# Kernel tuning notes

Measured on AMD Instinct MI355X. Metric: run time of the kernel, lower is better.

The kernel has to match this reference:

```python
import jax, jax.numpy as jnp
import numpy as np

N = 50000   # nodes
E = 300000  # directed edges
IN = 512
H = 256
OUT = 256
K = 4096    # K_target; since K < N, pooled node count Kc == K statically


def setup_inputs() -> dict:
    key = jax.random.key(0)
    ks = jax.random.split(key, 8)
    x = jax.random.normal(ks[0], (N, IN), jnp.float32)
    edge_index = jax.random.randint(ks[1], (2, E), 0, N)
    W1 = jax.random.normal(ks[2], (IN, H), jnp.float32) / np.float32(np.sqrt(IN))
    b1 = jnp.zeros((H,), jnp.float32)
    W2 = jax.random.normal(ks[3], (H, OUT), jnp.float32) / np.float32(np.sqrt(H))
    b2 = jnp.zeros((OUT,), jnp.float32)
    w_score = jax.random.normal(ks[4], (H,), jnp.float32) / np.float32(np.sqrt(H))
    W_skip = jax.random.normal(ks[5], (H, OUT), jnp.float32) / np.float32(np.sqrt(H))
    b_skip = jnp.zeros((OUT,), jnp.float32)
    return dict(x=x, edge_index=edge_index, W1=W1, b1=b1, W2=W2, b2=b2,
                w_score=w_score, W_skip=W_skip, b_skip=b_skip)


def _gcn_sparse(x, src, dst, W, b, n):
    # PyG GCNConv(add_self_loops=True, normalize=True): out = D^{-1/2}(A+I)D^{-1/2} x W + b,
    # degrees computed on dst after adding self loops.
    h = x @ W
    loop = jnp.arange(n)
    s = jnp.concatenate([src, loop])
    d = jnp.concatenate([dst, loop])
    deg = jax.ops.segment_sum(jnp.ones_like(d, h.dtype), d, num_segments=n)
    dinv = jnp.where(deg > 0, jax.lax.rsqrt(deg), 0.0)
    coef = (dinv[s] * dinv[d])[:, None]
    return jax.ops.segment_sum(h[s] * coef, d, num_segments=n) + b


def _forward(x, edge_index, W1, b1, W2, b2, w_score, W_skip, b_skip):
    n = x.shape[0]
    src, dst = edge_index[0], edge_index[1]

    # conv1 + relu (dropout is identity in eval mode)
    x1 = jax.nn.relu(_gcn_sparse(x, src, dst, W1, b1, n))
    raw = x1 @ w_score                       # [N] score (Linear, no bias)
    x1g = x1 * jnp.tanh(raw)[:, None]        # gated features

    # top-K node selection
    _, kept = jax.lax.top_k(raw, K)          # sorted descending, like torch.topk
    keep_mask = jnp.zeros((n,), bool).at[kept].set(True)
    deg = jax.ops.segment_sum(jnp.ones((src.shape[0],), jnp.int32), src, num_segments=n)

    # cluster ids: kept nodes get 0..K-1 in topk order
    cid = jnp.full((n,), -1, jnp.int32).at[kept].set(jnp.arange(K, dtype=jnp.int32))

    # non-kept nodes join the kept (undirected) neighbor with max degree;
    # encode (degree, -node_id) so segment_max picks max degree, tie-break smallest id
    s_all = jnp.concatenate([src, dst])
    t_all = jnp.concatenate([dst, src])
    cand = jnp.where(keep_mask[t_all], deg[t_all] * n + (n - 1 - t_all), -1)
    best = jax.ops.segment_max(cand, s_all, num_segments=n)  # empty segs -> int min
    has = best >= 0
    best_t = (n - 1) - jnp.where(has, best % n, 0)
    # global fallback: kept node with max degree (tie-break: earliest in topk order)
    enc_k = deg[kept] * K + (K - 1 - jnp.arange(K))
    bg = kept[jnp.argmax(enc_k)]
    cid = jnp.where(keep_mask, cid, jnp.where(has, cid[best_t], cid[bg]))

    # mean pooling per cluster (pool_by_partition)
    sums = jax.ops.segment_sum(x1g, cid, num_segments=K)
    cnt = jnp.maximum(jax.ops.segment_sum(jnp.ones((n,), x.dtype), cid, num_segments=K), 1.0)
    xp = sums / cnt[:, None]

    # pooled edges with dedup + self-pair removal, as dense KxK adjacency (rows = dst)
    cu, cv = cid[src], cid[dst]
    A = jnp.zeros((K, K), x.dtype).at[cv, cu].max((cu != cv).astype(x.dtype))
    Ahat = A + jnp.eye(K, dtype=x.dtype)
    di = jax.lax.rsqrt(Ahat.sum(axis=1))     # deg >= 1 from self loops
    An = di[:, None] * Ahat * di[None, :]

    # conv2 on pooled graph, broadcast back, skip connection
    xp2 = An @ (xp @ W2) + b2
    return xp2[cid] + x1 @ W_skip + b_skip


def reference(x, edge_index, W1, b1, W2, b2, w_score, W_skip, b_skip):
    return _forward(x, edge_index, W1, b1, W2, b2, w_score, W_skip, b_skip)
```

## Files before the change

### kernel.cpp

```cpp
#include <hip/hip_runtime.h>
#include <hip/hip_bf16.h>

#define N_NODES 50000
#define E_EDGES 300000
#define IN_F 512
#define H_F 256
#define OUT_F 256
#define K_CL 4096
#define KW (K_CL / 32)
#define PCH 128
#define THRESH 192
#define MAXH 1024
#define NSPL 32
#define NB2 ((N_NODES + 255) / 256)

typedef short bh8 __attribute__((ext_vector_type(8)));
typedef float f4 __attribute__((ext_vector_type(4)));
typedef unsigned short u16;

__device__ __forceinline__ unsigned fkey(float f) {
    unsigned u = __float_as_uint(f);
    return (u & 0x80000000u) ? ~u : (u | 0x80000000u);
}

__device__ __forceinline__ u16 f2bf(float f) {
    __hip_bfloat16 b = __float2bfloat16(f);
    return *reinterpret_cast<u16*>(&b);
}

__global__ __launch_bounds__(256) void init_nodes(int* cntD, int* degS,
                                                  unsigned long long* best_enc,
                                                  int* bgnode, int* heavycnt,
                                                  unsigned long long* bestpack) {
    int i = blockIdx.x * blockDim.x + threadIdx.x;
    if (i < N_NODES) { cntD[i] = 0; degS[i] = 0; best_enc[i] = 0ULL; }
    if (i == 0) { *heavycnt = 0; *bgnode = 0x7FFFFFFF; *bestpack = 0ULL; }
}

__global__ __launch_bounds__(256) void deg_edges(const int* __restrict__ src,
                                                 const int* __restrict__ dst,
                                                 int* cntD, int* degS) {
    int e = blockIdx.x * blockDim.x + threadIdx.x;
    if (e >= E_EDGES) return;
    atomicAdd(&cntD[dst[e]], 1);
    atomicAdd(&degS[src[e]], 1);
}

#define SBM 64
#define SBN 128
#define SBK 16
#define SAPAD 4
__global__ __launch_bounds__(256) void gemm_f32s(const float* __restrict__ A,
                                                 const float* __restrict__ B,
                                                 float* __restrict__ C,
                                                 int M, int Nc, int Kd) {
    __shared__ float As[2][SBK][SBM + SAPAD];
    __shared__ float Bs[2][SBK][SBN];
    int tid = threadIdx.x;
    int tx = tid & 15;
    int ty = tid >> 4;
    int lane = tid & 63;
    int wave = tid >> 6;
    int row0 = blockIdx.y * SBM, col0 = blockIdx.x * SBN;
    float acc[4][8] = {};

    int ar = tid >> 2;
    int akq = tid & 3;

    auto stage_B = [&](int k0, int bb) {
        #pragma unroll
        for (int u = 0; u < 2; ++u) {
            int chunk = wave * 2 + u;
            int krow = chunk * 2 + (lane >> 5);
            const float* gsrc = &B[(long)(k0 + krow) * Nc + col0 + (lane & 31) * 4];
            __builtin_amdgcn_global_load_lds(
                (const __attribute__((address_space(1))) void*)gsrc,
                (__attribute__((address_space(3))) void*)&Bs[bb][chunk * 2][0],
                16, 0, 0);
        }
    };
    auto stage_A = [&](int k0, int bb) {
        int gr = row0 + ar;
        float4 v = {0.f, 0.f, 0.f, 0.f};
        if (gr < M) v = *(const float4*)&A[(long)gr * Kd + k0 + akq * 4];
        As[bb][akq * 4 + 0][ar] = v.x;
        As[bb][akq * 4 + 1][ar] = v.y;
        As[bb][akq * 4 + 2][ar] = v.z;
        As[bb][akq * 4 + 3][ar] = v.w;
    };
    auto compute = [&](int bb) {
        #pragma unroll
        for (int k = 0; k < SBK; ++k) {
            float4 a0 = *(const float4*)&As[bb][k][ty * 4];
            float4 b0 = *(const float4*)&Bs[bb][k][tx * 4];
            float4 b1 = *(const float4*)&Bs[bb][k][tx * 4 + 64];
            float av[4] = {a0.x, a0.y, a0.z, a0.w};
            float bv[8] = {b0.x, b0.y, b0.z, b0.w, b1.x, b1.y, b1.z, b1.w};
            #pragma unroll
            for (int i = 0; i < 4; ++i)
                #pragma unroll
                for (int j = 0; j < 8; ++j)
                    acc[i][j] += av[i] * bv[j];
        }
    };

    stage_B(0, 0);
    stage_A(0, 0);
    __syncthreads();
    int nt = Kd / SBK;
    for (int t = 0; t < nt; ++t) {
        int cb = t & 1;
        if (t + 1 < nt) {
            stage_B(SBK * (t + 1), cb ^ 1);
            stage_A(SBK * (t + 1), cb ^ 1);
        }
        compute(cb);
        __syncthreads();
    }

    #pragma unroll
    for (int i = 0; i < 4; ++i) {
        int gr = row0 + ty * 4 + i;
        if (gr >= M) continue;
        float4 o0 = {acc[i][0], acc[i][1], acc[i][2], acc[i][3]};
        float4 o1 = {acc[i][4], acc[i][5], acc[i][6], acc[i][7]};
        *(float4*)&C[(long)gr * Nc + col0 + tx * 4] = o0;
        *(float4*)&C[(long)gr * Nc + col0 + 64 + tx * 4] = o1;
    }
}

__global__ __launch_bounds__(256) void pack_W2(const float* __restrict__ Wa, u16* Bpa,
                                               const float* __restrict__ Wb, u16* Bpb) {
    int k = blockIdx.x & 255;
    const float* W = (blockIdx.x < 256) ? Wa : Wb;
    u16* Bp = (blockIdx.x < 256) ? Bpa : Bpb;
    int col = threadIdx.x;
    int kb = k >> 5, g = (k >> 3) & 3, j = k & 7;
    Bp[(((long)(kb * 4 + g) * 256) + col) * 8 + j] = f2bf(W[(long)k * 256 + col]);
}

__global__ __launch_bounds__(256) void gemm_mfma(const u16* __restrict__ Ab,
                                                 const float* __restrict__ Af32,
                                                 const int* __restrict__ cnt,
                                                 const u16* __restrict__ Bp,
                                                 float* __restrict__ C,
                                                 int M,
                                                 const int* __restrict__ cid,
                                                 const float* __restrict__ xp2,
                                                 const float* __restrict__ bskip) {
    int tid = threadIdx.x;
    int w = tid >> 6, l = tid & 63;
    int lo16 = l & 15, hi4 = l >> 4;
    int arow = blockIdx.x * 64 + w * 16 + lo16;
    f4 acc[16];
    #pragma unroll
    for (int n = 0; n < 16; ++n) acc[n] = (f4){0.f, 0.f, 0.f, 0.f};

    float s = 1.f;
    if (Af32 && arow < M) s = 1.f / fmaxf((float)cnt[arow], 1.f);

    #pragma unroll
    for (int kb = 0; kb < 8; ++kb) {
        bh8 a = {0, 0, 0, 0, 0, 0, 0, 0};
        if (arow < M) {
            if (Af32) {
                float4 v0 = *(const float4*)&Af32[(long)arow * 256 + kb * 32 + hi4 * 8];
                float4 v1 = *(const float4*)&Af32[(long)arow * 256 + kb * 32 + hi4 * 8 + 4];
                u16 tmp[8] = {f2bf(v0.x * s), f2bf(v0.y * s), f2bf(v0.z * s), f2bf(v0.w * s),
                              f2bf(v1.x * s), f2bf(v1.y * s), f2bf(v1.z * s), f2bf(v1.w * s)};
                a = *(const bh8*)tmp;
            } else {
                a = *(const bh8*)&Ab[(long)arow * 256 + kb * 32 + hi4 * 8];
            }
        }
        const u16* bbase = &Bp[(((long)(kb * 4 + hi4)) * 256 + lo16) * 8];
        #pragma unroll
        for (int n = 0; n < 16; ++n) {
            bh8 b = *(const bh8*)&bbase[(long)n * 128];
            acc[n] = __builtin_amdgcn_mfma_f32_16x16x32_bf16(a, b, acc[n], 0, 0, 0);
        }
    }

    int orow0 = blockIdx.x * 64 + w * 16 + hi4 * 4;
    #pragma unroll
    for (int r = 0; r < 4; ++r) {
        int gr = orow0 + r;
        if (gr >= M) continue;
        long rb = (long)gr * 256;
        const float* xrow = cid ? (xp2 + (long)cid[gr] * 256) : nullptr;
        #pragma unroll
        for (int n = 0; n < 16; ++n) {
            int gc = n * 16 + lo16;
            float v = acc[n][r];
            if (cid) v += xrow[gc] + bskip[gc];
            C[rb + gc] = v;
        }
    }
}

__global__ __launch_bounds__(256) void scan_l1(const int* __restrict__ cnt,
                                               int* bsum, int n, float* dinv) {
    __shared__ int s[256];
    int t = threadIdx.x;
    int i = blockIdx.x * 256 + t;
    int v = (i < n) ? cnt[i] : 0;
    if (dinv && i < n) dinv[i] = rsqrtf((float)v + 1.0f);
    s[t] = v;
    __syncthreads();
    for (int off = 128; off > 0; off >>= 1) {
        if (t < off) s[t] += s[t + off];
        __syncthreads();
    }
    if (t == 0) bsum[blockIdx.x] = s[0];
}

__global__ __launch_bounds__(256) void scan_l2(const int* __restrict__ bsum,
                                               int* bstart, int nb) {
    __shared__ int s[256];
    int t = threadIdx.x;
    int v = (t < nb) ? bsum[t] : 0;
    s[t] = v;
    __syncthreads();
    for (int off = 1; off < 256; off <<= 1) {
        int a = (t >= off) ? s[t - off] : 0;
        __syncthreads();
        s[t] += a;
        __syncthreads();
    }
    if (t < nb) bstart[t] = s[t] - v;
}

__global__ __launch_bounds__(256) void scan_l3(const int* __restrict__ cnt,
                                               const int* __restrict__ bstart,
                                               int* start, int* cur, int n) {
    __shared__ int s[256];
    int t = threadIdx.x;
    int i = blockIdx.x * 256 + t;
    int v = (i < n) ? cnt[i] : 0;
    s[t] = v;
    __syncthreads();
    for (int off = 1; off < 256; off <<= 1) {
        int a = (t >= off) ? s[t - off] : 0;
        __syncthreads();
        s[t] += a;
        __syncthreads();
    }
    int st = bstart[blockIdx.x] + s[t] - v;
    if (i < n) { start[i] = st; cur[i] = st; }
    if (i == n - 1) start[n] = st + v;
}

__global__ __launch_bounds__(256) void csr_scatter(const int* __restrict__ src,
                                                   const int* __restrict__ dst,
                                                   int* cur, int* csr) {
    int e = blockIdx.x * blockDim.x + threadIdx.x;
    if (e >= E_EDGES) return;
    int d = dst[e];
    int p = atomicAdd(&cur[d], 1);
    csr[p] = src[e];
}

__global__ __launch_bounds__(256) void agg_fused(const float* __restrict__ h,
                                                 const float* __restrict__ dinv,
                                                 const int* __restrict__ rowptr,
                                                 const int* __restrict__ csr,
                                                 const float* __restrict__ b1,
                                                 const float* __restrict__ w_score,
                                                 float* x1, u16* x1b, float* raw) {
    __shared__ int s_src[128];
    __shared__ float s_cf[128];
    __shared__ float red[256];
    int i = blockIdx.x, j = threadIdx.x;
    float di_ = dinv[i];
    float acc = di_ * di_ * h[(long)i * H_F + j];
    int p0 = rowptr[i], p1 = rowptr[i + 1];
    for (int base = p0; base < p1; base += 128) {
        int m = p1 - base; if (m > 128) m = 128;
        if (j < m) { int s = csr[base + j]; s_src[j] = s; s_cf[j] = dinv[s]; }
        __syncthreads();
        #pragma unroll 4
        for (int t = 0; t < m; ++t)
            acc += (s_cf[t] * di_) * h[(long)s_src[t] * H_F + j];
        __syncthreads();
    }
    float v = fmaxf(acc + b1[j], 0.f);
    x1[(long)i * H_F + j] = v;
    x1b[(long)i * H_F + j] = f2bf(v);
    red[j] = v * w_score[j];
    __syncthreads();
    for (int off = 128; off > 0; off >>= 1) {
        if (j < off) red[j] += red[j + off];
        __syncthreads();
    }
    if (j == 0) raw[i] = red[0];
}

__global__ __launch_bounds__(1024) void topk_select(const float* __restrict__ raw,
                                                    unsigned* outT, int* outNeedEq) {
    __shared__ unsigned hist[256];
    __shared__ unsigned sh_prefix;
    __shared__ int sh_k;
    int tid = threadIdx.x;
    if (tid == 0) { sh_prefix = 0; sh_k = K_CL; }
    __syncthreads();
    for (int byte = 3; byte >= 0; --byte) {
        if (tid < 256) hist[tid] = 0;
        __syncthreads();
        unsigned prefix = sh_prefix;
        unsigned known_mask = (byte == 3) ? 0u : (0xFFFFFFFFu << ((byte + 1) * 8));
        for (int i = tid; i < N_NODES; i += 1024) {
            unsigned key = fkey(raw[i]);
            if ((key & known_mask) == prefix)
                atomicAdd(&hist[(key >> (byte * 8)) & 255], 1u);
        }
        __syncthreads();
        if (tid == 0) {
            int kk = sh_k;
            int cum = 0;
            int v = 255;
            for (; v > 0; --v) {
                int c = (int)hist[v];
                if (cum + c >= kk) break;
                cum += c;
            }
            sh_prefix = prefix | ((unsigned)v << (byte * 8));
            sh_k = kk - cum;
        }
        __syncthreads();
    }
    if (tid == 0) { *outT = sh_prefix; *outNeedEq = sh_k; }
}

__global__ __launch_bounds__(256) void topk_count(const float* __restrict__ raw,
                                                  const unsigned* pT,
                                                  int* bGt, int* bEq) {
    __shared__ int sg[256], se[256];
    unsigned T = *pT;
    int t = threadIdx.x;
    int i = blockIdx.x * 256 + t;
    int gt = 0, eq = 0;
    if (i < N_NODES) {
        unsigned k = fkey(raw[i]);
        gt = k > T; eq = (k == T);
    }
    sg[t] = gt; se[t] = eq;
    __syncthreads();
    for (int off = 128; off > 0; off >>= 1) {
        if (t < off) { sg[t] += sg[t + off]; se[t] += se[t + off]; }
        __syncthreads();
    }
    if (t == 0) { bGt[blockIdx.x] = sg[0]; bEq[blockIdx.x] = se[0]; }
}

__global__ __launch_bounds__(256) void scan_blocks(const int* __restrict__ bGt,
                                                   const int* __restrict__ bEq,
                                                   int* gtStart, int* eqStart) {
    __shared__ int sg[256], se[256];
    int t = threadIdx.x;
    int vg = (t < NB2) ? bGt[t] : 0;
    int ve = (t < NB2) ? bEq[t] : 0;
    sg[t] = vg; se[t] = ve;
    __syncthreads();
    for (int off = 1; off < 256; off <<= 1) {
        int a = (t >= off) ? sg[t - off] : 0;
        int b = (t >= off) ? se[t - off] : 0;
        __syncthreads();
        sg[t] += a; se[t] += b;
        __syncthreads();
    }
    if (t < NB2) { gtStart[t] = sg[t] - vg; eqStart[t] = se[t] - ve; }
    if (t == 255) gtStart[NB2] = sg[255];
}

__global__ __launch_bounds__(256) void topk_assign(const float* __restrict__ raw,
                                                   const unsigned* pT, const int* pNeedEq,
                                                   const int* __restrict__ degS,
                                                   const int* __restrict__ gtStart,
                                                   const int* __restrict__ eqStart,
                                                   int* keep, int* cid,
                                                   unsigned long long* bestpack) {
    __shared__ int sg[256], se[256];
    unsigned T = *pT;
    int needEq = *pNeedEq;
    int totalGt = gtStart[NB2];
    int b = blockIdx.x, t = threadIdx.x;
    int i = b * 256 + t;
    int gt = 0, eq = 0;
    unsigned k = 0;
    if (i < N_NODES) {
        k = fkey(raw[i]);
        gt = k > T; eq = (k == T);
    }
    sg[t] = gt; se[t] = eq;
    __syncthreads();
    for (int off = 1; off < 256; off <<= 1) {
        int a = (t >= off) ? sg[t - off] : 0;
        int c = (t >= off) ? se[t - off] : 0;
        __syncthreads();
        sg[t] += a; se[t] += c;
        __syncthreads();
    }
    int eg = sg[t] - gt, ee = se[t] - eq;
    int kp = 0;
    unsigned long long p = 0ULL;
    if (i < N_NODES) {
        int c = -1;
        if (gt) { kp = 1; c = gtStart[b] + eg; }
        else if (eq) {
            int r = eqStart[b] + ee;
            if (r < needEq) { kp = 1; c = totalGt + r; }
        }
        keep[i] = kp; cid[i] = c;
        if (kp) p = ((unsigned long long)(unsigned)degS[i] << 32) | k;
    }
    #pragma unroll
    for (int o = 32; o > 0; o >>= 1) {
        unsigned long long q = __shfl_xor((long long)p, o, 64);
        if (q > p) p = q;
    }
    if ((t & 63) == 0 && p) atomicMax(bestpack, p);
}

__global__ __launch_bounds__(256) void bg_node(const int* __restrict__ keep,
                                               const int* __restrict__ degS,
                                               const float* __restrict__ raw,
                                               const unsigned long long* bestpack, int* bgnode) {
    int i = blockIdx.x * blockDim.x + threadIdx.x;
    if (i < N_NODES && keep[i]) {
        unsigned long long p = ((unsigned long long)(unsigned)degS[i] << 32) | fkey(raw[i]);
        if (p == *bestpack) atomicMin(bgnode, i);
    }
}

__global__ __launch_bounds__(256) void neigh_edges(const int* __restrict__ src,
                                                   const int* __restrict__ dst,
                                                   const int* __restrict__ keep,
                                                   const int* __restrict__ degS,
                                                   unsigned long long* best_enc) {
    int e = blockIdx.x * blockDim.x + threadIdx.x;
    if (e >= 2 * E_EDGES) return;
    int s, t;
    if (e < E_EDGES) { s = src[e]; t = dst[e]; }
    else { s = dst[e - E_EDGES]; t = src[e - E_EDGES]; }
    if (!keep[s] && keep[t]) {
        unsigned long long enc =
            (unsigned long long)((long long)degS[t] * N_NODES + (N_NODES - 1 - t)) + 1ULL;
        atomicMax(&best_enc[s], enc);
    }
}

__global__ __launch_bounds__(256) void resolve_cid(const int* __restrict__ keep,
                                                   const unsigned long long* __restrict__ best_enc,
                                                   const int* __restrict__ bgnode, int* cid) {
    int i = blockIdx.x * blockDim.x + threadIdx.x;
    if (i >= N_NODES) return;
    if (keep[i]) return;
    unsigned long long v = best_enc[i];
    if (v > 0ULL) {
        long long enc = (long long)(v - 1ULL);
        int t = (N_NODES - 1) - (int)(enc % N_NODES);
        cid[i] = cid[t];
    } else {
        cid[i] = cid[*bgnode];
    }
}

#define NPB 1024
__global__ __launch_bounds__(256) void ccount2(const int* __restrict__ cid, int* ccnt) {
    __shared__ int hist[K_CL];
    for (int t = threadIdx.x; t < K_CL; t += 256) hist[t] = 0;
    __syncthreads();
    int base = blockIdx.x * NPB;
    #pragma unroll
    for (int u = 0; u < NPB / 256; ++u) {
        int idx = base + u * 256 + threadIdx.x;
        if (idx < N_NODES) atomicAdd(&hist[cid[idx]], 1);
    }
    __syncthreads();
    for (int t = threadIdx.x; t < K_CL; t += 256) {
        int hh = hist[t];
        if (hh) atomicAdd(&ccnt[t], hh);
    }
}

__global__ __launch_bounds__(256) void cscatter2(const int* __restrict__ cid,
                                                 int* ccur, int* clist) {
    __shared__ int hist[K_CL];
    for (int t = threadIdx.x; t < K_CL; t += 256) hist[t] = 0;
    __syncthreads();
    int base = blockIdx.x * NPB;
    int myc[NPB / 256], myr[NPB / 256];
    #pragma unroll
    for (int u = 0; u < NPB / 256; ++u) {
        int idx = base + u * 256 + threadIdx.x;
        if (idx < N_NODES) { myc[u] = cid[idx]; myr[u] = atomicAdd(&hist[myc[u]], 1); }
        else myc[u] = -1;
    }
    __syncthreads();
    for (int t = threadIdx.x; t < K_CL; t += 256) {
        int hh = hist[t];
        if (hh) hist[t] = atomicAdd(&ccur[t], hh);
    }
    __syncthreads();
    #pragma unroll
    for (int u = 0; u < NPB / 256; ++u)
        if (myc[u] >= 0) clist[hist[myc[u]] + myr[u]] = base + u * 256 + threadIdx.x;
}

__global__ __launch_bounds__(256) void pool_chunk(const float* __restrict__ x1,
                                                  const float* __restrict__ raw,
                                                  const int* __restrict__ clist,
                                                  const int* __restrict__ cid,
                                                  float* xp) {
    __shared__ int s_node[PCH];
    __shared__ int s_c[PCH];
    __shared__ float s_g[PCH];
    int j = threadIdx.x;
    int base = blockIdx.x * PCH;
    int m = N_NODES - base; if (m > PCH) m = PCH;
    for (int t = j; t < m; t += 256) {
        int nd = clist[base + t];
        s_node[t] = nd;
        s_c[t] = cid[nd];
        s_g[t] = tanhf(raw[nd]);
    }
    __syncthreads();
    float acc = 0.f;
    int cprev = s_c[0];
    for (int t = 0; t < m; t += 4) {
        int mm = m - t; if (mm > 4) mm = 4;
        float v[4];
        #pragma unroll
        for (int u = 0; u < 4; ++u)
            if (u < mm) v[u] = x1[(long)s_node[t + u] * H_F + j];
        #pragma unroll
        for (int u = 0; u < 4; ++u) {
            if (u < mm) {
                int c = s_c[t + u];
                if (c != cprev) {
                    atomicAdd(&xp[(long)cprev * H_F + j], acc);
                    acc = 0.f;
                    cprev = c;
                }
                acc += s_g[t + u] * v[u];
            }
        }
    }
    atomicAdd(&xp[(long)cprev * H_F + j], acc);
}

__global__ __launch_bounds__(256) void build_Abits(const int* __restrict__ src,
                                                   const int* __restrict__ dst,
                                                   const int* __restrict__ cid,
                                                   unsigned* Abits) {
    int e = blockIdx.x * blockDim.x + threadIdx.x;
    if (e >= E_EDGES) return;
    int cu = cid[src[e]], cv = cid[dst[e]];
    if (cu != cv) atomicOr(&Abits[(long)cv * KW + (cu >> 5)], 1u << (cu & 31));
}

__global__ __launch_bounds__(256) void pop_di2(const unsigned* __restrict__ Abits, float* di,
                                               int* nnzA, int* heavy, int* heavycnt) {
    int i = blockIdx.x * blockDim.x + threadIdx.x;
    if (i >= K_CL) return;
    int c = 0;
    for (int w = 0; w < KW; ++w) c += __popc(Abits[(long)i * KW + w]);
    di[i] = rsqrtf((float)c + 1.0f);
    nnzA[i] = c;
    if (c > THRESH) {
        int p = atomicAdd(heavycnt, 1);
        if (p < MAXH) heavy[p] = i;
    }
}

__global__ __launch_bounds__(256) void spmm_light(const unsigned* __restrict__ Abits,
                                                  const float* __restrict__ xpW2,
                                                  const float* __restrict__ di,
                                                  const float* __restrict__ b2,
                                                  const int* __restrict__ nnzA,
                                                  float* xp2) {
    __shared__ unsigned s_row[KW];
    __shared__ float s_part[3][256];
    int cv = blockIdx.x;
    if (nnzA[cv] > THRESH) return;
    int tid = threadIdx.x;
    int w = tid >> 6, l = tid & 63;
    if (tid < KW) s_row[tid] = Abits[(long)cv * KW + tid];
    __syncthreads();
    float4 a0 = {0.f, 0.f, 0.f, 0.f}, a1 = {0.f, 0.f, 0.f, 0.f};
    const float4* Y4 = (const float4*)xpW2;
    for (int wi = w * 32; wi < w * 32 + 32; wi += 2) {
        unsigned w0 = s_row[wi], w1 = s_row[wi + 1];
        while (w0 | w1) {
            if (w0) {
                int b = __ffs(w0) - 1; w0 &= w0 - 1;
                int cu = wi * 32 + b;
                float d = di[cu];
                float4 y = Y4[(long)cu * 64 + l];
                a0.x += d * y.x; a0.y += d * y.y; a0.z += d * y.z; a0.w += d * y.w;
            }
            if (w1) {
                int b = __ffs(w1) - 1; w1 &= w1 - 1;
                int cu = (wi + 1) * 32 + b;
                float d = di[cu];
                float4 y = Y4[(long)cu * 64 + l];
                a1.x += d * y.x; a1.y += d * y.y; a1.z += d * y.z; a1.w += d * y.w;
            }
        }
    }
    float4 acc = {a0.x + a1.x, a0.y + a1.y, a0.z + a1.z, a0.w + a1.w};
    if (w > 0) *(float4*)&s_part[w - 1][l * 4] = acc;
    __syncthreads();
    if (w == 0) {
        #pragma unroll
        for (int ww = 0; ww < 3; ++ww) {
            float4 p = *(float4*)&s_part[ww][l * 4];
            acc.x += p.x; acc.y += p.y; acc.z += p.z; acc.w += p.w;
        }
        float dv = di[cv];
        float4 ys = Y4[(long)cv * 64 + l];
        float4 o;
        o.x = dv * (acc.x + dv * ys.x) + b2[l * 4 + 0];
        o.y = dv * (acc.y + dv * ys.y) + b2[l * 4 + 1];
        o.z = dv * (acc.z + dv * ys.z) + b2[l * 4 + 2];
        o.w = dv * (acc.w + dv * ys.w) + b2[l * 4 + 3];
        *(float4*)&xp2[(long)cv * H_F + l * 4] = o;
    }
}

__global__ __launch_bounds__(256) void spmm_heavy(const unsigned* __restrict__ Abits,
                                                  const float* __restrict__ xpW2,
                                                  const float* __restrict__ di,
                                                  const int* __restrict__ heavy,
                                                  const int* __restrict__ heavycnt,
                                                  float* Zacc) {
    __shared__ float s_part[3][256];
    int hi = blockIdx.x;
    int cnt = *heavycnt; if (cnt > MAXH) cnt = MAXH;
    if (hi >= cnt) return;
    int cv = heavy[hi];
    int sp = blockIdx.y;
    int tid = threadIdx.x;
    int w = tid >> 6, l = tid & 63;
    int wi = sp * (KW / NSPL) + w;
    unsigned word = Abits[(long)cv * KW + wi];
    float4 acc = {0.f, 0.f, 0.f, 0.f};
    const float4* Y4 = (const float4*)xpW2;
    while (word) {
        int b = __ffs(word) - 1; word &= word - 1;
        int cu = wi * 32 + b;
        float d = di[cu];
        float4 y = Y4[(long)cu * 64 + l];
        acc.x += d * y.x; acc.y += d * y.y; acc.z += d * y.z; acc.w += d * y.w;
    }
    if (w > 0) *(float4*)&s_part[w - 1][l * 4] = acc;
    __syncthreads();
    if (w == 0) {
        #pragma unroll
        for (int ww = 0; ww < 3; ++ww) {
            float4 p = *(float4*)&s_part[ww][l * 4];
            acc.x += p.x; acc.y += p.y; acc.z += p.z; acc.w += p.w;
        }
        float* zp = &Zacc[(long)cv * H_F + l * 4];
        atomicAdd(zp + 0, acc.x);
        atomicAdd(zp + 1, acc.y);
        atomicAdd(zp + 2, acc.z);
        atomicAdd(zp + 3, acc.w);
    }
}

__global__ __launch_bounds__(256) void heavy_epi(const float* __restrict__ Zacc,
                                                 const float* __restrict__ xpW2,
                                                 const float* __restrict__ di,
                                                 const float* __restrict__ b2,
                                                 const int* __restrict__ heavy,
                                                 const int* __restrict__ heavycnt,
                                                 float* xp2) {
    int hi = blockIdx.x;
    int cnt = *heavycnt; if (cnt > MAXH) cnt = MAXH;
    if (hi >= cnt) return;
    int cv = heavy[hi];
    int j = threadIdx.x;
    float dv = di[cv];
    xp2[(long)cv * H_F + j] =
        dv * (Zacc[(long)cv * H_F + j] + dv * xpW2[(long)cv * H_F + j]) + b2[j];
}

static inline size_t align256(size_t x) { return (x + 255) & ~(size_t)255; }

extern "C" void kernel_launch(void* const* d_in, const int* in_sizes, int n_in,
                              void* d_out, int out_size, void* d_ws, size_t ws_size,
                              hipStream_t stream) {
    const float* x      = (const float*)d_in[0];
    const int*   eidx   = (const int*)d_in[1];
    const float* W1     = (const float*)d_in[2];
    const float* b1     = (const float*)d_in[3];
    const float* W2     = (const float*)d_in[4];
    const float* b2     = (const float*)d_in[5];
    const float* wscore = (const float*)d_in[6];
    const float* Wskip  = (const float*)d_in[7];
    const float* bskip  = (const float*)d_in[8];
    float* out = (float*)d_out;

    const int* src = eidx;
    const int* dst = eidx + E_EDGES;

    char* ws = (char*)d_ws;
    size_t off = 0;
    auto alloc = [&](size_t bytes) { char* p = ws + off; off += align256(bytes); return p; };

    float* h     = (float*)alloc((size_t)N_NODES * H_F * 4);
    float* x1    = (float*)alloc((size_t)N_NODES * H_F * 4);
    u16*   x1b   = (u16*)alloc((size_t)N_NODES * H_F * 2);
    float* raw   = (float*)alloc((size_t)N_NODES * 4);
    float* dinv  = (float*)alloc((size_t)N_NODES * 4);
    int*   cntD  = (int*)alloc((size_t)N_NODES * 4);
    int*   degS  = (int*)alloc((size_t)N_NODES * 4);
    int*   keep  = (int*)alloc((size_t)N_NODES * 4);
    int*   cid   = (int*)alloc((size_t)N_NODES * 4);
    unsigned long long* best_enc = (unsigned long long*)alloc((size_t)N_NODES * 8);
    int*   rowptr= (int*)alloc((size_t)(N_NODES + 1) * 4);
    int*   cur   = (int*)alloc((size_t)N_NODES * 4);
    int*   csr   = (int*)alloc((size_t)E_EDGES * 4);
    int*   ccnt  = (int*)alloc((size_t)K_CL * 4);
    int*   cstart= (int*)alloc((size_t)(K_CL + 1) * 4);
    int*   ccur  = (int*)alloc((size_t)K_CL * 4);
    int*   clist = (int*)alloc((size_t)N_NODES * 4);
    int*   bGt   = (int*)alloc((size_t)NB2 * 4);
    int*   bEq   = (int*)alloc((size_t)NB2 * 4);
    int*   gtStart = (int*)alloc((size_t)(NB2 + 1) * 4);
    int*   eqStart = (int*)alloc((size_t)NB2 * 4);
    int*   bsum  = (int*)alloc((size_t)256 * 4);
    int*   bstart= (int*)alloc((size_t)256 * 4);
    char*  small = alloc(64);
    unsigned* selT = (unsigned*)(small + 0);
    int* needEq    = (int*)(small + 4);
    int* bgnode    = (int*)(small + 8);
    int* heavycnt  = (int*)(small + 12);
    unsigned long long* bestpack = (unsigned long long*)(small + 16);
    float* xp    = (float*)alloc((size_t)K_CL * H_F * 4);
    unsigned* Abits = (unsigned*)alloc((size_t)K_CL * KW * 4);
    float* di    = (float*)alloc((size_t)K_CL * 4);
    int*   nnzA  = (int*)alloc((size_t)K_CL * 4);
    int*   heavy = (int*)alloc((size_t)MAXH * 4);
    float* Zacc  = (float*)alloc((size_t)K_CL * H_F * 4);
    float* xpW2  = (float*)alloc((size_t)K_CL * H_F * 4);
    float* xp2   = (float*)alloc((size_t)K_CL * H_F * 4);
    u16*  BpS   = (u16*)alloc((size_t)H_F * OUT_F * 2);
    u16*  Bp2   = (u16*)alloc((size_t)H_F * H_F * 2);
    (void)ws_size; (void)n_in; (void)in_sizes; (void)out_size;

    int nb = NB2;
    int eb = (E_EDGES + 255) / 256;

    init_nodes<<<nb, 256, 0, stream>>>(cntD, degS, best_enc, bgnode, heavycnt, bestpack);
    deg_edges<<<eb, 256, 0, stream>>>(src, dst, cntD, degS);

    pack_W2<<<512, 256, 0, stream>>>(Wskip, BpS, W2, Bp2);

    {
        dim3 grid(H_F / SBN, (N_NODES + SBM - 1) / SBM);
        gemm_f32s<<<grid, 256, 0, stream>>>(x, W1, h, N_NODES, H_F, IN_F);
    }

    scan_l1<<<NB2, 256, 0, stream>>>(cntD, bsum, N_NODES, dinv);
    scan_l2<<<1, 256, 0, stream>>>(bsum, bstart, NB2);
    scan_l3<<<NB2, 256, 0, stream>>>(cntD, bstart, rowptr, cur, N_NODES);
    csr_scatter<<<eb, 256, 0, stream>>>(src, dst, cur, csr);
    agg_fused<<<N_NODES, 256, 0, stream>>>(h, dinv, rowptr, csr, b1, wscore, x1, x1b, raw);

    topk_select<<<1, 1024, 0, stream>>>(raw, selT, needEq);
    topk_count<<<NB2, 256, 0, stream>>>(raw, selT, bGt, bEq);
    scan_blocks<<<1, 256, 0, stream>>>(bGt, bEq, gtStart, eqStart);
    topk_assign<<<NB2, 256, 0, stream>>>(raw, selT, needEq, degS, gtStart, eqStart,
                                         keep, cid, bestpack);
    bg_node<<<nb, 256, 0, stream>>>(keep, degS, raw, bestpack, bgnode);

    neigh_edges<<<(2 * E_EDGES + 255) / 256, 256, 0, stream>>>(src, dst, keep, degS, best_enc);
    resolve_cid<<<nb, 256, 0, stream>>>(keep, best_enc, bgnode, cid);

    hipMemsetAsync(ccnt, 0, (size_t)K_CL * 4, stream);
    {
        int cb = (N_NODES + NPB - 1) / NPB;
        ccount2<<<cb, 256, 0, stream>>>(cid, ccnt);
        scan_l1<<<K_CL / 256, 256, 0, stream>>>(ccnt, bsum, K_CL, nullptr);
        scan_l2<<<1, 256, 0, stream>>>(bsum, bstart, K_CL / 256);
        scan_l3<<<K_CL / 256, 256, 0, stream>>>(ccnt, bstart, cstart, ccur, K_CL);
        cscatter2<<<cb, 256, 0, stream>>>(cid, ccur, clist);
    }
    hipMemsetAsync(xp, 0, (size_t)K_CL * H_F * 4, stream);
    pool_chunk<<<(N_NODES + PCH - 1) / PCH, 256, 0, stream>>>(x1, raw, clist, cid, xp);

    gemm_mfma<<<K_CL / 64, 256, 0, stream>>>(nullptr, xp, ccnt, Bp2, xpW2, K_CL,
                                             nullptr, nullptr, nullptr);

    hipMemsetAsync(Abits, 0, (size_t)K_CL * KW * 4, stream);
    hipMemsetAsync(Zacc, 0, (size_t)K_CL * H_F * 4, stream);
    build_Abits<<<eb, 256, 0, stream>>>(src, dst, cid, Abits);
    pop_di2<<<(K_CL + 255) / 256, 256, 0, stream>>>(Abits, di, nnzA, heavy, heavycnt);
    spmm_light<<<K_CL, 256, 0, stream>>>(Abits, xpW2, di, b2, nnzA, xp2);
    {
        dim3 hgrid(MAXH, NSPL);
        spmm_heavy<<<hgrid, 256, 0, stream>>>(Abits, xpW2, di, heavy, heavycnt, Zacc);
    }
    heavy_epi<<<MAXH, 256, 0, stream>>>(Zacc, xpW2, di, b2, heavy, heavycnt, xp2);

    gemm_mfma<<<(N_NODES + 63) / 64, 256, 0, stream>>>(x1b, nullptr, nullptr, BpS, out,
                                                       N_NODES, cid, xp2, bskip);
}
```

Before: 727.8 us.

## Stage fp32 GEMM A tile via direct-to-LDS loads with XOR swizzle; merge memsets

The first FP32 GEMM (x @ W1) now loads the A tile straight into shared memory with global_load_lds. It uses a row-major XOR-swizzled layout instead of transposing through registers, and the compute loop reads A as float4 per row to match. Separately, buffers are reordered so xp, Abits and Zacc sit next to each other and can be cleared with one memset. This is meant to cut register traffic and instruction overhead in the large GEMM and to save memset launches. The risks are LDS bank conflicts from the new access pattern and the contiguity assumption that the single memset relies on.

Result: no change. 721.3 us (-0.9%).

```diff
diff --git a/kernel.cpp b/kernel.cpp
--- a/kernel.cpp
+++ b/kernel.cpp
@@ -49,12 +49,11 @@
 #define SBM 64
 #define SBN 128
 #define SBK 16
-#define SAPAD 4
 __global__ __launch_bounds__(256) void gemm_f32s(const float* __restrict__ A,
                                                  const float* __restrict__ B,
                                                  float* __restrict__ C,
                                                  int M, int Nc, int Kd) {
-    __shared__ float As[2][SBK][SBM + SAPAD];
+    __shared__ float As[2][SBM][SBK];
     __shared__ float Bs[2][SBK][SBN];
     int tid = threadIdx.x;
     int tx = tid & 15;
@@ -64,8 +63,8 @@
     int row0 = blockIdx.y * SBM, col0 = blockIdx.x * SBN;
     float acc[4][8] = {};
 
-    int ar = tid >> 2;
-    int akq = tid & 3;
+    int arow = wave * 16 + (lane >> 2);
+    int acolf = ((((lane & 3) * 16) ^ (((lane >> 4) & 1) << 5)) >> 2);
 
     auto stage_B = [&](int k0, int bb) {
         #pragma unroll
@@ -80,27 +79,37 @@
         }
     };
     auto stage_A = [&](int k0, int bb) {
-        int gr = row0 + ar;
-        float4 v = {0.f, 0.f, 0.f, 0.f};
-        if (gr < M) v = *(const float4*)&A[(long)gr * Kd + k0 + akq * 4];
-        As[bb][akq * 4 + 0][ar] = v.x;
-        As[bb][akq * 4 + 1][ar] = v.y;
-        As[bb][akq * 4 + 2][ar] = v.z;
-        As[bb][akq * 4 + 3][ar] = v.w;
+        int gr = row0 + arow;
+        if (gr > M - 1) gr = M - 1;
+        const float* gsrc = &A[(long)gr * Kd + k0 + acolf];
+        __builtin_amdgcn_global_load_lds(
+            (const __attribute__((address_space(1))) void*)gsrc,
+            (__attribute__((address_space(3))) void*)&As[bb][wave * 16][0],
+            16, 0, 0);
     };
     auto compute = [&](int bb) {
         #pragma unroll
-        for (int k = 0; k < SBK; ++k) {
-            float4 a0 = *(const float4*)&As[bb][k][ty * 4];
-            float4 b0 = *(const float4*)&Bs[bb][k][tx * 4];
-            float4 b1 = *(const float4*)&Bs[bb][k][tx * 4 + 64];
-            float av[4] = {a0.x, a0.y, a0.z, a0.w};
-            float bv[8] = {b0.x, b0.y, b0.z, b0.w, b1.x, b1.y, b1.z, b1.w};
+        for (int kq = 0; kq < 4; ++kq) {
+            float4 af[4];
             #pragma unroll
-            for (int i = 0; i < 4; ++i)
+            for (int i = 0; i < 4; ++i) {
+                int row = ty * 4 + i;
+                int cb = ((kq * 16 ^ (((row >> 2) & 1) << 5)) >> 2);
+                af[i] = *(const float4*)&As[bb][row][cb];
+            }
+            #pragma unroll
+            for (int kk = 0; kk < 4; ++kk) {
+                int k = kq * 4 + kk;
+                float4 b0 = *(const float4*)&Bs[bb][k][tx * 4];
+                float4 b1 = *(const float4*)&Bs[bb][k][tx * 4 + 64];
+                float bv[8] = {b0.x, b0.y, b0.z, b0.w, b1.x, b1.y, b1.z, b1.w};
+                float av[4] = {af[0][kk], af[1][kk], af[2][kk], af[3][kk]};
                 #pragma unroll
-                for (int j = 0; j < 8; ++j)
-                    acc[i][j] += av[i] * bv[j];
+                for (int i = 0; i < 4; ++i)
+                    #pragma unroll
+                    for (int j = 0; j < 8; ++j)
+                        acc[i][j] += av[i] * bv[j];
+            }
         }
     };
 
@@ -740,10 +749,10 @@
     unsigned long long* bestpack = (unsigned long long*)(small + 16);
     float* xp    = (float*)alloc((size_t)K_CL * H_F * 4);
     unsigned* Abits = (unsigned*)alloc((size_t)K_CL * KW * 4);
+    float* Zacc  = (float*)alloc((size_t)K_CL * H_F * 4);
     float* di    = (float*)alloc((size_t)K_CL * 4);
     int*   nnzA  = (int*)alloc((size_t)K_CL * 4);
     int*   heavy = (int*)alloc((size_t)MAXH * 4);
-    float* Zacc  = (float*)alloc((size_t)K_CL * H_F * 4);
     float* xpW2  = (float*)alloc((size_t)K_CL * H_F * 4);
     float* xp2   = (float*)alloc((size_t)K_CL * H_F * 4);
     u16*  BpS   = (u16*)alloc((size_t)H_F * OUT_F * 2);
@@ -778,6 +787,8 @@
 
     neigh_edges<<<(2 * E_EDGES + 255) / 256, 256, 0, stream>>>(src, dst, keep, degS, best_enc);
     resolve_cid<<<nb, 256, 0, stream>>>(keep, best_enc, bgnode, cid);
+
+    hipMemsetAsync(xp, 0, (size_t)K_CL * H_F * 4 * 2 + (size_t)K_CL * KW * 4, stream);
 
     hipMemsetAsync(ccnt, 0, (size_t)K_CL * 4, stream);
     {
@@ -788,14 +799,11 @@
         scan_l3<<<K_CL / 256, 256, 0, stream>>>(ccnt, bstart, cstart, ccur, K_CL);
         cscatter2<<<cb, 256, 0, stream>>>(cid, ccur, clist);
     }
-    hipMemsetAsync(xp, 0, (size_t)K_CL * H_F * 4, stream);
     pool_chunk<<<(N_NODES + PCH - 1) / PCH, 256, 0, stream>>>(x1, raw, clist, cid, xp);
 
     gemm_mfma<<<K_CL / 64, 256, 0, stream>>>(nullptr, xp, ccnt, Bp2, xpW2, K_CL,
                                              nullptr, nullptr, nullptr);
 
-    hipMemsetAsync(Abits, 0, (size_t)K_CL * KW * 4, stream);
-    hipMemsetAsync(Zacc, 0, (size_t)K_CL * H_F * 4, stream);
     build_Abits<<<eb, 256, 0, stream>>>(src, dst, cid, Abits);
     pop_di2<<<(K_CL + 255) / 256, 256, 0, stream>>>(Abits, di, nnzA, heavy, heavycnt);
     spmm_light<<<K_CL, 256, 0, stream>>>(Abits, xpW2, di, b2, nnzA, xp2);
```
